# Kernel optimization log

Hardware: AMD Instinct MI355X
Metric: run time of the kernel (lower is better)

## Reference

```python
import jax, jax.numpy as jnp
import numpy as np

# HBV parameter bounds, in the order of self.parameters_bound
BOUNDS = np.array([
    [1.0, 6.0],     # parBETA
    [50.0, 1000.0], # parFC
    [0.05, 0.9],    # parK0
    [0.01, 0.5],    # parK1
    [0.001, 0.2],   # parK2
    [0.2, 1.0],     # parLP
    [0.0, 10.0],    # parPERC
    [0.0, 100.0],   # parUZL
    [-2.5, 2.5],    # parTT
    [0.5, 10.0],    # parCFMAX
    [0.0, 0.1],     # parCFR
    [0.0, 0.2],     # parCWH
    [0.3, 5.0],     # parBETAET
    [0.0, 1.0],     # parC (capillary)
    [0.0, 20.0],    # parTRbound (unused in core recurrence)
    [0.0, 2500.0],  # parAc (unused in core recurrence)
], dtype=np.float32)
NEARZERO = 1e-5
LENF = 15  # unit-hydrograph length
ROUT_A_MAX = 2.9
ROUT_B_MAX = 6.5


def uh_gamma(a, b, lenF):
    # a, b: [Ngrid]; returns normalized gamma UH weights [lenF, Ngrid]
    aa = jax.nn.relu(a) + 0.1
    theta = jax.nn.relu(b) + 0.5
    tt = jnp.arange(0.5, float(lenF), dtype=jnp.float32)[:, None]  # [lenF,1]
    w = jnp.exp(-jax.scipy.special.gammaln(aa)) / (theta ** aa) * tt ** (aa - 1.0) * jnp.exp(-tt / theta)
    return w / w.sum(0)


def hbv_forward(x_hydro_model, params_raw, conv_params_hydro):
    # x_hydro_model: [T, N, 3] (P, Temp, PET); params_raw: [T, N, 16, M]; conv: [N, 2]
    T, N, _ = x_hydro_model.shape
    M = params_raw.shape[-1]
    b = jnp.asarray(BOUNDS)
    p = b[:, 0].reshape(1, 1, -1, 1) + params_raw * (b[:, 1] - b[:, 0]).reshape(1, 1, -1, 1)
    (BETA, FC, K0, K1, K2, LP, PERC, UZL, TT, CFMAX, CFR, CWH, BETAET, C) = [p[:, :, i, :] for i in range(14)]
    Pm = x_hydro_model[:, :, 0:1]    # [T,N,1] broadcast vs nmul
    Tm = x_hydro_model[:, :, 1:2]
    PETm = x_hydro_model[:, :, 2:3]

    init = tuple(jnp.full((N, M), 0.001, jnp.float32) for _ in range(5))

    def step(carry, inp):
        SNOWPACK, MELTWATER, SM, SUZ, SLZ = carry
        (P_, Ta, PET_, BETA_, FC_, K0_, K1_, K2_, LP_, PERC_, UZL_, TT_, CFMAX_, CFR_, CWH_, BETAET_, C_) = inp
        RAIN = jnp.where(Ta >= TT_, P_, 0.0)
        SNOW = jnp.where(Ta < TT_, P_, 0.0)
        # snow routine
        SNOWPACK = SNOWPACK + SNOW
        melt = jnp.minimum(jnp.maximum(CFMAX_ * (Ta - TT_), 0.0), SNOWPACK)
        MELTWATER = MELTWATER + melt
        SNOWPACK = jnp.maximum(SNOWPACK - melt, NEARZERO)
        refreeze = jnp.minimum(jnp.maximum(CFR_ * CFMAX_ * (TT_ - Ta), 0.0), MELTWATER)
        SNOWPACK = SNOWPACK + refreeze
        MELTWATER = jnp.maximum(MELTWATER - refreeze, NEARZERO)
        tosoil = jnp.maximum(MELTWATER - CWH_ * SNOWPACK, 0.0)
        MELTWATER = jnp.maximum(MELTWATER - tosoil, NEARZERO)
        # soil routine
        soil_wet = jnp.clip((SM / FC_) ** BETA_, 0.0, 1.0)
        recharge = (RAIN + tosoil) * soil_wet
        SM = SM + RAIN + tosoil - recharge
        excess = jnp.maximum(SM - FC_, 0.0)
        SM = jnp.maximum(SM - excess, NEARZERO)
        evapfactor = jnp.clip((SM / (LP_ * FC_)) ** BETAET_, 0.0, 1.0)
        ETact = jnp.minimum(SM, PET_ * evapfactor)
        SM = jnp.maximum(SM - ETact, NEARZERO)
        # capillary rise from lower zone (parC)
        capillary = jnp.minimum(SLZ, C_ * SLZ * (1.0 - jnp.minimum(SM / FC_, 1.0)))
        SM = SM + capillary
        SLZ = jnp.maximum(SLZ - capillary, NEARZERO)
        # response routine
        SUZ = SUZ + recharge + excess
        PERCa = jnp.minimum(SUZ, PERC_)
        SUZ = SUZ - PERCa
        Q0 = K0_ * jnp.maximum(SUZ - UZL_, 0.0)
        SUZ = SUZ - Q0
        Q1 = K1_ * SUZ
        SUZ = SUZ - Q1
        SLZ = SLZ + PERCa
        Q2 = K2_ * SLZ
        SLZ = SLZ - Q2
        Qt = (Q0 + Q1 + Q2).mean(-1)  # average over nmul components -> [N]
        return (SNOWPACK, MELTWATER, SM, SUZ, SLZ), Qt

    _, Qsim = jax.lax.scan(step, init, (Pm, Tm, PETm, BETA, FC, K0, K1, K2, LP, PERC, UZL, TT, CFMAX, CFR, CWH, BETAET, C))
    # gamma-UH routing (causal per-grid convolution)
    rout_a = conv_params_hydro[:, 0] * ROUT_A_MAX
    rout_b = conv_params_hydro[:, 1] * ROUT_B_MAX
    UH = uh_gamma(rout_a, rout_b, LENF)  # [LENF, N]
    Qpad = jnp.pad(Qsim, ((LENF - 1, 0), (0, 0)))  # [T+LENF-1, N]
    Qrout = jnp.zeros_like(Qsim)
    for k in range(LENF):  # small fixed kernel length
        Qrout = Qrout + UH[k][None, :] * Qpad[LENF - 1 - k: LENF - 1 - k + T]
    return Qrout  # [T, N]


def setup_inputs() -> dict:
    key = jax.random.key(0)
    k1, k2, k3, k4, k5 = jax.random.split(key, 5)
    T, N, NP, M = 365, 4000, 16, 4
    P = jax.random.uniform(k1, (T, N), jnp.float32) * 15.0        # precip mm/day
    Temp = jax.random.uniform(k2, (T, N), jnp.float32) * 35.0 - 10.0  # deg C
    PET = jax.random.uniform(k3, (T, N), jnp.float32) * 6.0       # mm/day
    x_hydro_model = jnp.stack([P, Temp, PET], axis=-1)             # [T,N,3]
    params_raw = jax.random.uniform(k4, (T, N, NP, M), jnp.float32)
    conv_params_hydro = jax.random.uniform(k5, (N, 2), jnp.float32)
    return {"x_hydro_model": x_hydro_model, "params_raw": params_raw, "conv_params_hydro": conv_params_hydro}


def reference(x_hydro_model, params_raw, conv_params_hydro):
    return hbv_forward(x_hydro_model, params_raw, conv_params_hydro)
```

## Files before the change

### kernel.cpp

```cpp
#include <hip/hip_runtime.h>
#include <math.h>

#define NEARZERO 1e-5f
#define LENF 15

#define KB 8
#define FORC_OFS (KB * 1024)
#define BUF_BYTES 8704
#define LDS_BYTES (2 * BUF_BYTES)

#define WAIT_VMCNT_9  0x0F79
#define WAIT_VMCNT_17 0x4F71
#define WAIT_LGKM_0   0xC07F

#define GPTR(p) ((const __attribute__((address_space(1))) void*)(p))
#define LPTR(p) ((__attribute__((address_space(3))) void*)(p))

__device__ __forceinline__ float qswap1(float v) {
    return __int_as_float(__builtin_amdgcn_update_dpp(
        0, __float_as_int(v), 0xB1 , 0xF, 0xF, true));
}
__device__ __forceinline__ float qswap2(float v) {
    return __int_as_float(__builtin_amdgcn_update_dpp(
        0, __float_as_int(v), 0x4E , 0xF, 0xF, true));
}

__device__ __forceinline__ float powpos(float x, float y) {
    return __builtin_amdgcn_exp2f(y * __builtin_amdgcn_logf(x));
}
__device__ __forceinline__ float rcpf(float x) { return __builtin_amdgcn_rcpf(x); }

__device__ __forceinline__ void stage_batch(const char* __restrict__ praw_b,
                                            const char* __restrict__ x_b,
                                            char* smem, int buf, int t0,
                                            int T, int N, int n0, int lane,
                                            int perm16, int s3, int k16)
{
    char* bufp = smem + buf * BUF_BYTES;
#pragma unroll
    for (int s = 0; s < KB; ++s) {
        int ts = t0 + s;
        if (ts > T - 1) ts = T - 1;
        const char* gp = praw_b + (size_t)ts * ((size_t)N * 256) + (size_t)n0 * 256;
        __builtin_amdgcn_global_load_lds(GPTR(gp + perm16),
                                         LPTR(bufp + s * 1024), 16, 0, 0);
    }
    if (lane < 24) {
        int ts = t0 + s3;
        if (ts > T - 1) ts = T - 1;
        const char* xg = x_b + (size_t)ts * ((size_t)N * 12) + (size_t)n0 * 12;
        __builtin_amdgcn_global_load_lds(GPTR(xg + k16),
                                         LPTR(bufp + FORC_OFS), 16, 0, 0);
    }
}

__device__ __forceinline__ float dostep(const float* __restrict__ pr,
                                        float P, float Ta, float PET,
                                        float& SNOWPACK, float& MELTWATER,
                                        float& SM, float& SUZ, float& SLZ)
{
    const float BETA   = fmaf(pr[0],  5.0f,   1.0f);
    const float FC     = fmaf(pr[1],  950.0f, 50.0f);
    const float K0     = fmaf(pr[2],  0.85f,  0.05f);
    const float K1     = fmaf(pr[3],  0.49f,  0.01f);
    const float K2     = fmaf(pr[4],  0.199f, 0.001f);
    const float LP     = fmaf(pr[5],  0.8f,   0.2f);
    const float PERC   = pr[6] * 10.0f;
    const float UZL    = pr[7] * 100.0f;
    const float TT     = __fadd_rn(-2.5f, __fmul_rn(pr[8], 5.0f));
    const float CFMAX  = fmaf(pr[9],  9.5f,   0.5f);
    const float CFR    = pr[10] * 0.1f;
    const float CWH    = pr[11] * 0.2f;
    const float BETAET = fmaf(pr[12], 4.7f,   0.3f);
    const float C      = pr[13];

    const bool  wet  = (Ta >= TT);
    const float RAIN = wet ? P : 0.0f;
    const float SNOW = wet ? 0.0f : P;

    SNOWPACK += SNOW;
    const float melt = fminf(fmaxf(CFMAX * (Ta - TT), 0.0f), SNOWPACK);
    MELTWATER += melt;
    SNOWPACK = fmaxf(SNOWPACK - melt, NEARZERO);
    const float refreeze = fminf(fmaxf(CFR * CFMAX * (TT - Ta), 0.0f), MELTWATER);
    SNOWPACK += refreeze;
    MELTWATER = fmaxf(MELTWATER - refreeze, NEARZERO);
    const float tosoil = fmaxf(MELTWATER - CWH * SNOWPACK, 0.0f);
    MELTWATER = fmaxf(MELTWATER - tosoil, NEARZERO);

    const float rFC = rcpf(FC);
    float soil_wet = powpos(SM * rFC, BETA);
    soil_wet = fminf(fmaxf(soil_wet, 0.0f), 1.0f);
    const float recharge = (RAIN + tosoil) * soil_wet;
    SM = SM + RAIN + tosoil - recharge;
    const float excess = fmaxf(SM - FC, 0.0f);
    SM = fmaxf(SM - excess, NEARZERO);

    float evapfactor = powpos(SM * rcpf(LP * FC), BETAET);
    evapfactor = fminf(fmaxf(evapfactor, 0.0f), 1.0f);
    const float ETact = fminf(SM, PET * evapfactor);
    SM = fmaxf(SM - ETact, NEARZERO);

    const float capillary = fminf(SLZ, C * SLZ * (1.0f - fminf(SM * rFC, 1.0f)));
    SM += capillary;
    SLZ = fmaxf(SLZ - capillary, NEARZERO);

    SUZ = SUZ + recharge + excess;
    const float PERCa = fminf(SUZ, PERC);
    SUZ -= PERCa;
    const float Q0 = K0 * fmaxf(SUZ - UZL, 0.0f);
    SUZ -= Q0;
    const float Q1 = K1 * SUZ;
    SUZ -= Q1;
    SLZ += PERCa;
    const float Q2 = K2 * SLZ;
    SLZ -= Q2;
    return Q0 + Q1 + Q2;
}

__device__ __forceinline__ void make_uh(float craw0, float craw1, float* UH)
{
    const float a  = craw0 * 2.9f;
    const float b  = craw1 * 6.5f;
    const float aa = fmaxf(a, 0.0f) + 0.1f;
    const float th = fmaxf(b, 0.0f) + 0.5f;
    const float L2E = 1.4426950408889634f;
    const float c   = -lgammaf(aa) * L2E - aa * __builtin_amdgcn_logf(th);
    const float rthL = rcpf(th) * L2E;
    float wsum = 0.0f;
#pragma unroll
    for (int k = 0; k < LENF; ++k) {
        const float tt   = (float)k + 0.5f;
        const float l2tt = __builtin_log2f((float)k + 0.5f);
        const float l2w  = fmaf(aa - 1.0f, l2tt, c) - tt * rthL;
        UH[k] = __builtin_amdgcn_exp2f(l2w);
        wsum += UH[k];
    }
    const float rs = rcpf(wsum);
#pragma unroll
    for (int k = 0; k < LENF; ++k) UH[k] *= rs;
}

__global__ void __launch_bounds__(64, 1)
hbv_kernel(const float* __restrict__ x,
           const float* __restrict__ praw,
           const float* __restrict__ conv,
           float* __restrict__ out,
           int T, int N)
{
    __shared__ __align__(16) char smem[LDS_BYTES];

    const int lane = threadIdx.x;
    int n0 = blockIdx.x * 4;
    if (n0 > N - 4) n0 = N - 4;
    const int nl = (lane >> 2) & 3;
    const int m  = lane & 3;
    const int n  = n0 + nl;
    const int perm16 = (lane ^ ((lane >> 3) & 6)) << 4;
    const int s3  = lane / 3;
    const int k16 = (lane - 3 * s3) * 16;

    const int q0 = nl & 1, q1 = (nl >> 1) & 1;
    char* pp[4];
#pragma unroll
    for (int j = 0; j < 4; ++j) {
        const int d = 64 * (((j >> 1) & 1) ^ q1) + 32 * ((j & 1) ^ q0);
        pp[j] = smem + nl * 256 + m * 4 + d;
    }
    char* pf = smem + FORC_OFS + 12 * nl;

    float UH[LENF];
    make_uh(conv[2 * n], conv[2 * n + 1], UH);

    float acc[LENF - 1];
#pragma unroll
    for (int k = 0; k < LENF - 1; ++k) acc[k] = 0.0f;

    float S0 = 0.001f, S1 = 0.001f, S2 = 0.001f, S3v = 0.001f, S4 = 0.001f;

    const char* praw_b = (const char*)praw;
    const char* x_b    = (const char*)x;

    stage_batch(praw_b, x_b, smem, 0, 0,  T, N, n0, lane, perm16, s3, k16);
    stage_batch(praw_b, x_b, smem, 1, KB, T, N, n0, lane, perm16, s3, k16);

    float pA[14], fA[3], pB[14], fB[3];

#define LOADSLOT(P, F, S)                                                     \
    {                                                                         \
        _Pragma("unroll")                                                     \
        for (int i = 0; i < 14; ++i) {                                        \
            const int j = 2 * ((i >> 2) & 1) + ((i >> 1) & 1);                \
            const int o = (S) * 1024 + 128 * (i >> 3) + 16 * (i & 1);         \
            P[i] = *(const float*)(pp[j] + o);                                \
        }                                                                     \
        _Pragma("unroll")                                                     \
        for (int k = 0; k < 3; ++k)                                           \
            F[k] = *(const float*)(pf + (S) * 48 + 4 * k);                    \
    }

#define STEPT(P, F, TIDX)                                                     \
    {                                                                         \
        float v = dostep(P, F[0], F[1], F[2], S0, S1, S2, S3v, S4);           \
        v += qswap1(v);                                                       \
        v += qswap2(v);                                                       \
        const float qq = v * 0.25f;                                           \
        const float e = fmaf(UH[0], qq, acc[0]);                              \
        _Pragma("unroll")                                                     \
        for (int k = 0; k < LENF - 2; ++k)                                    \
            acc[k] = fmaf(UH[k + 1], qq, acc[k + 1]);                         \
        acc[LENF - 2] = UH[LENF - 1] * qq;                                    \
        if ((lane & 0x33) == 0)       \
            out[(size_t)(TIDX) * N + n] = e;                                  \
    }

    __builtin_amdgcn_s_waitcnt(WAIT_VMCNT_9);
    __builtin_amdgcn_sched_barrier(0);

    int dl = BUF_BYTES;
    int t = 0;
    const int nb = T / KB;
    for (int bb = 0; bb < nb; ++bb) {
        __builtin_amdgcn_s_waitcnt(WAIT_VMCNT_17);
        __builtin_amdgcn_sched_barrier(0);

        LOADSLOT(pA, fA, 0);
        LOADSLOT(pB, fB, 1);
        STEPT(pA, fA, t + 0);
        LOADSLOT(pA, fA, 2);
        STEPT(pB, fB, t + 1);
        LOADSLOT(pB, fB, 3);
        STEPT(pA, fA, t + 2);
        LOADSLOT(pA, fA, 4);
        STEPT(pB, fB, t + 3);
        LOADSLOT(pB, fB, 5);
        STEPT(pA, fA, t + 4);
        LOADSLOT(pA, fA, 6);
        STEPT(pB, fB, t + 5);
        LOADSLOT(pB, fB, 7);
        STEPT(pA, fA, t + 6);
        STEPT(pB, fB, t + 7);
        t += KB;

        __builtin_amdgcn_s_waitcnt(WAIT_LGKM_0);
        __builtin_amdgcn_sched_barrier(0);
        stage_batch(praw_b, x_b, smem, bb & 1, (bb + 2) * KB, T, N, n0, lane,
                    perm16, s3, k16);
#pragma unroll
        for (int j = 0; j < 4; ++j) pp[j] += dl;
        pf += dl; dl = -dl;
    }

    if (t < T) {
        __builtin_amdgcn_s_waitcnt(WAIT_VMCNT_17);
        __builtin_amdgcn_sched_barrier(0);
        for (int s = 0; s < KB && t < T; ++s, ++t) {
            LOADSLOT(pA, fA, s);
            STEPT(pA, fA, t);
        }
    }
#undef LOADSLOT
#undef STEPT
}

extern "C" void kernel_launch(void* const* d_in, const int* in_sizes, int n_in,
                              void* d_out, int out_size, void* d_ws, size_t ws_size,
                              hipStream_t stream)
{
    const float* x    = (const float*)d_in[0];
    const float* praw = (const float*)d_in[1];
    const float* conv = (const float*)d_in[2];
    float* out = (float*)d_out;

    const int N = in_sizes[2] / 2;
    const int T = in_sizes[0] / (3 * N);

    const int grid = (N + 3) / 4;
    hipLaunchKernelGGL(hbv_kernel, dim3(grid), dim3(64), 0, stream,
                       x, praw, conv, out, T, N);
}
```

Before: 544.6 us.

## Map 16 grid cells per wavefront to use all lanes, with padded LDS chunks

Each 64-lane wave now processes 16 grid cells instead of 4, so all lanes do distinct work rather than 48 lanes duplicating the same cells, and the grid shrinks fourfold. Staging now loads four 1 KB parameter chunks per timestep into LDS chunks padded to 1040 bytes, which is meant to reduce bank conflicts. Forcing loads become per-lane 4-byte transfers. The batch depth drops from 8 to 7 timesteps and the vmcnt waits are adjusted to match. The risk is that far fewer waves are resident, so memory latency is hidden less well across the GPU.

```diff
diff --git a/kernel.cpp b/kernel.cpp
--- a/kernel.cpp
+++ b/kernel.cpp
@@ -4,13 +4,18 @@
 #define NEARZERO 1e-5f
 #define LENF 15
 
-#define KB 8
-#define FORC_OFS (KB * 1024)
-#define BUF_BYTES 8704
-#define LDS_BYTES (2 * BUF_BYTES)
-
-#define WAIT_VMCNT_9  0x0F79
-#define WAIT_VMCNT_17 0x4F71
+#define KB 7
+#define CHUNK_BYTES 1040
+#define CHUNK_WORDS 260
+#define SLOT_PARAM_B (4 * CHUNK_BYTES)
+#define SLOT_PARAM_W (4 * CHUNK_WORDS)
+#define SLOT_BYTES (SLOT_PARAM_B + 256)
+#define SLOT_WORDS (SLOT_BYTES / 4)
+#define BUF_BYTES (KB * SLOT_BYTES)
+#define BUF_WORDS (KB * SLOT_WORDS)
+#define LDS_WORDS (2 * BUF_WORDS)
+
+#define WAIT_VMCNT_35 0x8F73
 #define WAIT_LGKM_0   0xC07F
 
 #define GPTR(p) ((const __attribute__((address_space(1))) void*)(p))
@@ -32,25 +37,28 @@
 
 __device__ __forceinline__ void stage_batch(const char* __restrict__ praw_b,
                                             const char* __restrict__ x_b,
-                                            char* smem, int buf, int t0,
+                                            float* smemf, int buf, int t0,
                                             int T, int N, int n0, int lane,
-                                            int perm16, int s3, int k16)
-{
-    char* bufp = smem + buf * BUF_BYTES;
-#pragma unroll
+                                            int perm16)
+{
+    char* bufp = (char*)smemf + buf * BUF_BYTES;
     for (int s = 0; s < KB; ++s) {
         int ts = t0 + s;
         if (ts > T - 1) ts = T - 1;
         const char* gp = praw_b + (size_t)ts * ((size_t)N * 256) + (size_t)n0 * 256;
-        __builtin_amdgcn_global_load_lds(GPTR(gp + perm16),
-                                         LPTR(bufp + s * 1024), 16, 0, 0);
-    }
-    if (lane < 24) {
-        int ts = t0 + s3;
-        if (ts > T - 1) ts = T - 1;
+        char* sp = bufp + s * SLOT_BYTES;
+#pragma unroll
+        for (int c = 0; c < 4; ++c) {
+            __builtin_amdgcn_global_load_lds(GPTR(gp + c * 1024 + perm16),
+                                             LPTR(sp + c * CHUNK_BYTES),
+                                             16, 0, 0);
+        }
         const char* xg = x_b + (size_t)ts * ((size_t)N * 12) + (size_t)n0 * 12;
-        __builtin_amdgcn_global_load_lds(GPTR(xg + k16),
-                                         LPTR(bufp + FORC_OFS), 16, 0, 0);
+        if ((lane & 3) != 3) {
+            __builtin_amdgcn_global_load_lds(
+                GPTR(xg + 4 * (3 * (lane >> 2) + (lane & 3))),
+                LPTR(sp + SLOT_PARAM_B), 4, 0, 0);
+        }
     }
 }
 
@@ -148,26 +156,25 @@
            float* __restrict__ out,
            int T, int N)
 {
-    __shared__ __align__(16) char smem[LDS_BYTES];
+    __shared__ __align__(16) float smemf[LDS_WORDS];
 
     const int lane = threadIdx.x;
-    int n0 = blockIdx.x * 4;
-    if (n0 > N - 4) n0 = N - 4;
-    const int nl = (lane >> 2) & 3;
+    int n0 = blockIdx.x * 16;
+    if (n0 > N - 16) n0 = N - 16;
+    const int nl = lane >> 2;
     const int m  = lane & 3;
     const int n  = n0 + nl;
     const int perm16 = (lane ^ ((lane >> 3) & 6)) << 4;
-    const int s3  = lane / 3;
-    const int k16 = (lane - 3 * s3) * 16;
-
-    const int q0 = nl & 1, q1 = (nl >> 1) & 1;
-    char* pp[4];
-#pragma unroll
-    for (int j = 0; j < 4; ++j) {
-        const int d = 64 * (((j >> 1) & 1) ^ q1) + 32 * ((j & 1) ^ q0);
-        pp[j] = smem + nl * 256 + m * 4 + d;
-    }
-    char* pf = smem + FORC_OFS + 12 * nl;
+
+    const int a  = nl >> 2;
+    const int q  = nl & 3;
+    const int q0 = q & 1, q1 = (q >> 1) & 1;
+    int pb[4];
+#pragma unroll
+    for (int j = 0; j < 4; ++j)
+        pb[j] = a * CHUNK_WORDS + q * 64 + m
+              + 16 * (((j >> 1) & 1) ^ q1) + 8 * ((j & 1) ^ q0);
+    int fb = SLOT_PARAM_W + 4 * nl;
 
     float UH[LENF];
     make_uh(conv[2 * n], conv[2 * n + 1], UH);
@@ -181,8 +188,8 @@
     const char* praw_b = (const char*)praw;
     const char* x_b    = (const char*)x;
 
-    stage_batch(praw_b, x_b, smem, 0, 0,  T, N, n0, lane, perm16, s3, k16);
-    stage_batch(praw_b, x_b, smem, 1, KB, T, N, n0, lane, perm16, s3, k16);
+    stage_batch(praw_b, x_b, smemf, 0, 0,  T, N, n0, lane, perm16);
+    stage_batch(praw_b, x_b, smemf, 1, KB, T, N, n0, lane, perm16);
 
     float pA[14], fA[3], pB[14], fB[3];
 
@@ -191,12 +198,11 @@
         _Pragma("unroll")                                                     \
         for (int i = 0; i < 14; ++i) {                                        \
             const int j = 2 * ((i >> 2) & 1) + ((i >> 1) & 1);                \
-            const int o = (S) * 1024 + 128 * (i >> 3) + 16 * (i & 1);         \
-            P[i] = *(const float*)(pp[j] + o);                                \
+            P[i] = smemf[pb[j] + (S) * SLOT_WORDS + 32 * (i >> 3) + 4 * (i & 1)]; \
         }                                                                     \
         _Pragma("unroll")                                                     \
         for (int k = 0; k < 3; ++k)                                           \
-            F[k] = *(const float*)(pf + (S) * 48 + 4 * k);                    \
+            F[k] = smemf[fb + (S) * SLOT_WORDS + k];                          \
     }
 
 #define STEPT(P, F, TIDX)                                                     \
@@ -210,18 +216,14 @@
         for (int k = 0; k < LENF - 2; ++k)                                    \
             acc[k] = fmaf(UH[k + 1], qq, acc[k + 1]);                         \
         acc[LENF - 2] = UH[LENF - 1] * qq;                                    \
-        if ((lane & 0x33) == 0)       \
-            out[(size_t)(TIDX) * N + n] = e;                                  \
-    }
-
-    __builtin_amdgcn_s_waitcnt(WAIT_VMCNT_9);
-    __builtin_amdgcn_sched_barrier(0);
-
-    int dl = BUF_BYTES;
+        if (m == 0) out[(size_t)(TIDX) * N + n] = e;                          \
+    }
+
+    int dw = BUF_WORDS;
     int t = 0;
     const int nb = T / KB;
     for (int bb = 0; bb < nb; ++bb) {
-        __builtin_amdgcn_s_waitcnt(WAIT_VMCNT_17);
+        __builtin_amdgcn_s_waitcnt(WAIT_VMCNT_35);
         __builtin_amdgcn_sched_barrier(0);
 
         LOADSLOT(pA, fA, 0);
@@ -237,22 +239,20 @@
         STEPT(pA, fA, t + 4);
         LOADSLOT(pA, fA, 6);
         STEPT(pB, fB, t + 5);
-        LOADSLOT(pB, fB, 7);
         STEPT(pA, fA, t + 6);
-        STEPT(pB, fB, t + 7);
         t += KB;
 
         __builtin_amdgcn_s_waitcnt(WAIT_LGKM_0);
         __builtin_amdgcn_sched_barrier(0);
-        stage_batch(praw_b, x_b, smem, bb & 1, (bb + 2) * KB, T, N, n0, lane,
-                    perm16, s3, k16);
-#pragma unroll
-        for (int j = 0; j < 4; ++j) pp[j] += dl;
-        pf += dl; dl = -dl;
+        stage_batch(praw_b, x_b, smemf, bb & 1, (bb + 2) * KB, T, N, n0, lane,
+                    perm16);
+#pragma unroll
+        for (int j = 0; j < 4; ++j) pb[j] += dw;
+        fb += dw; dw = -dw;
     }
 
     if (t < T) {
-        __builtin_amdgcn_s_waitcnt(WAIT_VMCNT_17);
+        __builtin_amdgcn_s_waitcnt(WAIT_VMCNT_35);
         __builtin_amdgcn_sched_barrier(0);
         for (int s = 0; s < KB && t < T; ++s, ++t) {
             LOADSLOT(pA, fA, s);
@@ -275,7 +275,7 @@
     const int N = in_sizes[2] / 2;
     const int T = in_sizes[0] / (3 * N);
 
-    const int grid = (N + 3) / 4;
+    const int grid = (N + 15) / 16;
     hipLaunchKernelGGL(hbv_kernel, dim3(grid), dim3(64), 0, stream,
                        x, praw, conv, out, T, N);
 }
```

After: 502.5 us. 7.7% less time.
